# Optimization experiments

Measured on AMD Instinct MI355X. Metric: run time of the kernel, lower is better.

The kernel has to match this reference:

```python
import jax, jax.numpy as jnp
import numpy as np

N_NODES = 100000
N_EDGES = 1600000
D_FEAT = 128
N_CLASSES = 2
K_HOPS = 2


def setup_inputs() -> dict:
    key = jax.random.key(0)
    k1, k2, k3, k4 = jax.random.split(key, 4)
    x = jax.random.normal(k1, (N_NODES, D_FEAT), dtype=jnp.float32)
    edge_index = jax.random.randint(k2, (2, N_EDGES), 0, N_NODES, dtype=jnp.int64)
    weight = jax.random.normal(k3, (N_CLASSES, D_FEAT), dtype=jnp.float32) * (1.0 / np.sqrt(D_FEAT))
    bias = jnp.zeros((N_CLASSES,), dtype=jnp.float32)
    return {"x": x, "edge_index": edge_index, "weight": weight, "bias": bias}


def reference(x, edge_index, weight, bias):
    N = x.shape[0]
    # gcn_norm with self-loops (PyG SGConv default)
    loop = jnp.arange(N, dtype=edge_index.dtype)
    row = jnp.concatenate([edge_index[0], loop])  # source nodes
    col = jnp.concatenate([edge_index[1], loop])  # target nodes
    ones = jnp.ones(row.shape[0], dtype=x.dtype)
    deg = jax.ops.segment_sum(ones, col, num_segments=N)
    dinv = jnp.where(deg > 0, jax.lax.rsqrt(deg), 0.0)
    norm = dinv[row] * dinv[col]  # [E+N]

    # K hops of normalized sparse propagation: x <- A_norm @ x
    for _ in range(K_HOPS):
        x = jax.ops.segment_sum(x[row] * norm[:, None], col, num_segments=N)

    logits = x @ weight.T + bias  # [N, num_classes]
    return jax.nn.log_softmax(logits, axis=1)
```

## Files before the change

kernel.cpp:

```cpp
#include <hip/hip_runtime.h>

#define D_FEAT 128
#define BSH    8
#define BNODES 256
#define MAXNB  400
#define NSEG   512
#define SEGCAP 16
#define SENT   0xFFFFFFFFu
#define OVPB   16
#define MVB    2048
#define HTB    1024

typedef unsigned u32x4 __attribute__((ext_vector_type(4)));

__global__ __launch_bounds__(256) void k_fused(const float* __restrict__ x,
                                               const int* __restrict__ row,
                                               const int* __restrict__ col,
                                               const float* __restrict__ w,
                                               unsigned long long* __restrict__ ovbuf,
                                               unsigned* __restrict__ gbuf,
                                               float2* __restrict__ zvec,
                                               int E, int n, int NB) {
    __shared__ unsigned lcnt[MAXNB];
    __shared__ unsigned lbuf[MAXNB * SEGCAP];
    __shared__ unsigned lov;
    const int blk = blockIdx.x, tid = threadIdx.x;

    if (blk < NSEG) {
        for (int i = tid; i < NB; i += 256) lcnt[i] = 0;
        if (tid == 0) lov = 0;
        __syncthreads();

        const int chunk = (E + NSEG - 1) / NSEG;
        const int s = blk * chunk;
        const int e_end = min(s + chunk, E);
        for (int e = s + tid; e < e_end; e += 256) {
            int r = row[e], c = col[e];
            int b = c >> BSH;
            unsigned pos = atomicAdd(&lcnt[b], 1u);
            if (pos < SEGCAP) {
                lbuf[b * SEGCAP + pos] = ((unsigned)r << BSH) | (unsigned)(c & (BNODES - 1));
            } else {
                unsigned gi = atomicAdd(&lov, 1u);
                if (gi < OVPB)
                    ovbuf[(size_t)blk * OVPB + gi] =
                        ((unsigned long long)(unsigned)r << 32) | (unsigned)c;
            }
        }
        __syncthreads();

        if (tid < OVPB) {
            unsigned used = lov; if (used > OVPB) used = OVPB;
            if ((unsigned)tid >= used)
                ovbuf[(size_t)blk * OVPB + tid] = ~0ull;
        }

        const int total4 = NB * (SEGCAP / 4);
        uint4* g4 = (uint4*)gbuf;
        for (int idx = tid; idx < total4; idx += 256) {
            int b = idx >> 2, sg = (idx & 3) * 4;
            unsigned c2 = lcnt[b]; if (c2 > SEGCAP) c2 = SEGCAP;
            const unsigned* lb = &lbuf[b * SEGCAP + sg];
            uint4 v;
            v.x = ((unsigned)(sg + 0) < c2) ? lb[0] : SENT;
            v.y = ((unsigned)(sg + 1) < c2) ? lb[1] : SENT;
            v.z = ((unsigned)(sg + 2) < c2) ? lb[2] : SENT;
            v.w = ((unsigned)(sg + 3) < c2) ? lb[3] : SENT;
            g4[(((size_t)b * NSEG + blk) * SEGCAP + sg) >> 2] = v;
        }
    } else {
        const int lane = tid & 63;
        const float2 w0 = *(const float2*)(w + 2 * lane);
        const float2 w1 = *(const float2*)(w + D_FEAT + 2 * lane);
        const int wave0 = ((blk - NSEG) * 256 + tid) >> 6;
        const int nwaves = (MVB * 256) >> 6;
        for (int node = wave0; node < n; node += nwaves) {
            const float2 xv = *(const float2*)(x + (size_t)node * D_FEAT + 2 * lane);
            float p0 = xv.x * w0.x + xv.y * w0.y;
            float p1 = xv.x * w1.x + xv.y * w1.y;
            #pragma unroll
            for (int off = 32; off > 0; off >>= 1) {
                p0 += __shfl_down(p0, off, 64);
                p1 += __shfl_down(p1, off, 64);
            }
            if (lane == 0) zvec[node] = make_float2(p0, p1);
        }
    }
}

__global__ __launch_bounds__(HTB) void k_degnode(const unsigned* __restrict__ gbuf,
                                                 const unsigned long long* __restrict__ ovbuf,
                                                 const float2* __restrict__ z,
                                                 float* __restrict__ dinv,
                                                 float2* __restrict__ zd, int n) {
    __shared__ unsigned hist[BNODES];
    const int b = blockIdx.x, tid = threadIdx.x;
    if (tid < BNODES) hist[tid] = 0u;
    __syncthreads();

    const u32x4* p4 = (const u32x4*)(gbuf + (size_t)b * NSEG * SEGCAP);
    const int NIT = (NSEG * SEGCAP / 4) / HTB;
    #pragma unroll
    for (int k = 0; k < NIT; ++k) {
        u32x4 v = __builtin_nontemporal_load(p4 + tid + k * HTB);
        #pragma unroll
        for (int q = 0; q < 4; ++q)
            if (v[q] != SENT) atomicAdd(&hist[v[q] & (BNODES - 1)], 1u);
    }
    const int OVTOT = NSEG * OVPB;
    for (int i = tid; i < OVTOT; i += HTB) {
        unsigned long long e = ovbuf[i];
        unsigned c = (unsigned)e;
        if ((int)(c >> BSH) == b) atomicAdd(&hist[c & (BNODES - 1)], 1u);
    }
    __syncthreads();

    if (tid < BNODES) {
        int c = (b << BSH) + tid;
        if (c < n) {
            float d = rsqrtf((float)hist[tid] + 1.0f);
            dinv[c] = d;
            float2 zi = z[c];
            zd[c] = make_float2(zi.x * d, zi.y * d);
        }
    }
}

__global__ __launch_bounds__(HTB) void k_hop(const unsigned* __restrict__ gbuf,
                                             const unsigned long long* __restrict__ ovbuf,
                                             const float2* __restrict__ vin,
                                             const float* __restrict__ dinv,
                                             const float* __restrict__ bias,
                                             float2* __restrict__ outv,
                                             int n, int mode) {
    __shared__ float accx[BNODES];
    __shared__ float accy[BNODES];
    const int b = blockIdx.x, tid = threadIdx.x;
    if (tid < BNODES) { accx[tid] = 0.f; accy[tid] = 0.f; }
    __syncthreads();

    const u32x4* p4 = (const u32x4*)(gbuf + (size_t)b * NSEG * SEGCAP);
    const int NIT = (NSEG * SEGCAP / 4) / HTB;
    u32x4 vv[NIT];
    #pragma unroll
    for (int k = 0; k < NIT; ++k)
        vv[k] = __builtin_nontemporal_load(p4 + tid + k * HTB);

    #pragma unroll
    for (int k = 0; k < NIT; ++k) {
        u32x4 v = vv[k];
        #pragma unroll
        for (int q = 0; q < 4; ++q) {
            unsigned ent = v[q];
            if (ent != SENT) {
                float2 s = vin[ent >> BSH];
                atomicAdd(&accx[ent & (BNODES - 1)], s.x);
                atomicAdd(&accy[ent & (BNODES - 1)], s.y);
            }
        }
    }

    const int OVTOT = NSEG * OVPB;
    for (int i = tid; i < OVTOT; i += HTB) {
        unsigned long long e = ovbuf[i];
        unsigned c = (unsigned)e;
        if ((int)(c >> BSH) == b) {
            float2 s = vin[e >> 32];
            atomicAdd(&accx[c & (BNODES - 1)], s.x);
            atomicAdd(&accy[c & (BNODES - 1)], s.y);
        }
    }
    __syncthreads();

    if (tid < BNODES) {
        int c = (b << BSH) + tid;
        if (c < n) {
            float d = dinv[c];
            float2 s = vin[c];
            float ax = s.x + accx[tid];
            float ay = s.y + accy[tid];
            if (mode == 0) {
                float dd = d * d;
                outv[c] = make_float2(ax * dd, ay * dd);
            } else {
                float l0 = ax * d + bias[0];
                float l1 = ay * d + bias[1];
                float mx = fmaxf(l0, l1);
                float lse = mx + logf(expf(l0 - mx) + expf(l1 - mx));
                outv[c] = make_float2(l0 - lse, l1 - lse);
            }
        }
    }
}


__global__ __launch_bounds__(256) void k_matvec(const float* __restrict__ x,
                                                const float* __restrict__ w,
                                                float2* __restrict__ z, int n) {
    int wave = (int)((blockIdx.x * blockDim.x + threadIdx.x) >> 6);
    int lane = threadIdx.x & 63;
    if (wave >= n) return;
    const float2 xv = *(const float2*)(x + (size_t)wave * D_FEAT + 2 * lane);
    const float2 w0 = *(const float2*)(w + 2 * lane);
    const float2 w1 = *(const float2*)(w + D_FEAT + 2 * lane);
    float p0 = xv.x * w0.x + xv.y * w0.y;
    float p1 = xv.x * w1.x + xv.y * w1.y;
    #pragma unroll
    for (int off = 32; off > 0; off >>= 1) {
        p0 += __shfl_down(p0, off, 64);
        p1 += __shfl_down(p1, off, 64);
    }
    if (lane == 0) z[wave] = make_float2(p0, p1);
}

__global__ __launch_bounds__(256) void k_deg(const int* __restrict__ col,
                                             unsigned int* __restrict__ deg, int E) {
    int e = blockIdx.x * blockDim.x + threadIdx.x;
    if (e < E) atomicAdd(&deg[col[e]], 1u);
}

__global__ __launch_bounds__(256) void k_dinv_init(const unsigned int* __restrict__ deg,
                                                   float* __restrict__ dinv,
                                                   const float2* __restrict__ zin,
                                                   float2* __restrict__ yout, int n) {
    int i = blockIdx.x * blockDim.x + threadIdx.x;
    if (i < n) {
        float d = rsqrtf((float)deg[i] + 1.0f);
        dinv[i] = d;
        float2 zi = zin[i];
        float dd = d * d;
        yout[i] = make_float2(zi.x * dd, zi.y * dd);
    }
}

__global__ __launch_bounds__(256) void k_selfloop(const float* __restrict__ dinv,
                                                  const float2* __restrict__ zin,
                                                  float2* __restrict__ yout, int n) {
    int i = blockIdx.x * blockDim.x + threadIdx.x;
    if (i < n) {
        float d = dinv[i];
        float dd = d * d;
        float2 zi = zin[i];
        yout[i] = make_float2(zi.x * dd, zi.y * dd);
    }
}

__global__ __launch_bounds__(256) void k_edge(const int* __restrict__ row,
                                              const int* __restrict__ col,
                                              const float* __restrict__ dinv,
                                              const float2* __restrict__ zin,
                                              float* __restrict__ yout, int E) {
    int e = blockIdx.x * blockDim.x + threadIdx.x;
    if (e < E) {
        int r = row[e], c = col[e];
        float nr = dinv[r] * dinv[c];
        float2 zr = zin[r];
        atomicAdd(&yout[2 * c + 0], zr.x * nr);
        atomicAdd(&yout[2 * c + 1], zr.y * nr);
    }
}

__global__ __launch_bounds__(256) void k_final(const float2* __restrict__ y,
                                               const float* __restrict__ bias,
                                               float2* __restrict__ out, int n) {
    int i = blockIdx.x * blockDim.x + threadIdx.x;
    if (i < n) {
        float2 l = y[i];
        float l0 = l.x + bias[0];
        float l1 = l.y + bias[1];
        float m = fmaxf(l0, l1);
        float lse = m + logf(expf(l0 - m) + expf(l1 - m));
        out[i] = make_float2(l0 - lse, l1 - lse);
    }
}

extern "C" void kernel_launch(void* const* d_in, const int* in_sizes, int n_in,
                              void* d_out, int out_size, void* d_ws, size_t ws_size,
                              hipStream_t stream) {
    const float* x    = (const float*)d_in[0];
    const int*   ei   = (const int*)d_in[1];
    const float* w    = (const float*)d_in[2];
    const float* bias = (const float*)d_in[3];

    const int n = in_sizes[0] / D_FEAT;
    const int E = in_sizes[1] / 2;
    const int* row = ei;
    const int* col = ei + E;

    const int TB = 256;
    const int nodeBlocks = (n + TB - 1) / TB;
    const int edgeBlocks = (E + TB - 1) / TB;
    const int waveBlocks = (n + 3) / 4;

    const int NB = (n + BNODES - 1) >> BSH;

    size_t need = (size_t)NSEG * OVPB * 8
                + (size_t)NB * NSEG * SEGCAP * 4
                + (size_t)n * 8 * 3
                + (size_t)n * 4;

    if (NB <= MAXNB && n < (1 << 24) && ws_size >= need) {
        char* ws = (char*)d_ws;
        unsigned long long* ovbuf = (unsigned long long*)ws; ws += (size_t)NSEG * OVPB * 8;
        unsigned* gbuf = (unsigned*)ws;                      ws += (size_t)NB * NSEG * SEGCAP * 4;
        float2* zvec   = (float2*)ws;                        ws += (size_t)n * 8;
        float2* zd     = (float2*)ws;                        ws += (size_t)n * 8;
        float2* y1d    = (float2*)ws;                        ws += (size_t)n * 8;
        float*  dinv   = (float*)ws;

        k_fused  <<<NSEG + MVB, TB, 0, stream>>>(x, row, col, w, ovbuf, gbuf,
                                                 zvec, E, n, NB);
        k_degnode<<<NB, HTB, 0, stream>>>(gbuf, ovbuf, zvec, dinv, zd, n);
        k_hop    <<<NB, HTB, 0, stream>>>(gbuf, ovbuf, zd, dinv, bias, y1d, n, 0);
        k_hop    <<<NB, HTB, 0, stream>>>(gbuf, ovbuf, y1d, dinv, bias,
                                          (float2*)d_out, n, 1);
    } else {
        char* ws = (char*)d_ws;
        float2* z   = (float2*)ws; ws += (size_t)n * sizeof(float2);
        float2* y1  = (float2*)ws; ws += (size_t)n * sizeof(float2);
        float2* y2  = (float2*)ws; ws += (size_t)n * sizeof(float2);
        float*  dinv = (float*)ws; ws += (size_t)n * sizeof(float);
        unsigned int* deg = (unsigned int*)ws;

        (void)hipMemsetAsync(deg, 0, (size_t)n * sizeof(unsigned int), stream);
        k_deg<<<edgeBlocks, TB, 0, stream>>>(col, deg, E);
        k_matvec<<<waveBlocks, TB, 0, stream>>>(x, w, z, n);
        k_dinv_init<<<nodeBlocks, TB, 0, stream>>>(deg, dinv, z, y1, n);
        k_edge<<<edgeBlocks, TB, 0, stream>>>(row, col, dinv, z, (float*)y1, E);
        k_selfloop<<<nodeBlocks, TB, 0, stream>>>(dinv, y1, y2, n);
        k_edge<<<edgeBlocks, TB, 0, stream>>>(row, col, dinv, y1, (float*)y2, E);
        k_final<<<nodeBlocks, TB, 0, stream>>>(y2, bias, (float2*)d_out, n);
    }
}
```

Before: 165.6 us.

## Fuse bucketing, degree and both hops into one cooperative kernel

Replaces the four kernel launches with a single cooperative kernel of NB blocks that uses grid-wide syncs between the bucketing/matvec, degree, and two propagation phases. The edge partitioning now uses NB segments instead of a fixed 512, with segment capacity and overflow slots per segment enlarged to match. This removes the inter-kernel launch gaps and the tail effects of separate launches. In exchange it runs on only NB blocks of 512 threads (about 391), so parallelism in the bucketing and hop phases is lower, and it adds grid barrier costs. Overflow capacity is still bounded, so correctness depends on per-segment bucket counts staying within the new limits.

```diff
diff --git a/kernel.cpp b/kernel.cpp
--- a/kernel.cpp
+++ b/kernel.cpp
@@ -1,79 +1,92 @@
 #include <hip/hip_runtime.h>
+#include <hip/hip_cooperative_groups.h>
+
+namespace cg = cooperative_groups;
 
 #define D_FEAT 128
 #define BSH    8
 #define BNODES 256
 #define MAXNB  400
-#define NSEG   512
-#define SEGCAP 16
+#define SEGCAP 20
 #define SENT   0xFFFFFFFFu
-#define OVPB   16
-#define MVB    2048
-#define HTB    1024
+#define OVPB   32
+#define CTB    512
 
 typedef unsigned u32x4 __attribute__((ext_vector_type(4)));
 
-__global__ __launch_bounds__(256) void k_fused(const float* __restrict__ x,
-                                               const int* __restrict__ row,
-                                               const int* __restrict__ col,
-                                               const float* __restrict__ w,
-                                               unsigned long long* __restrict__ ovbuf,
-                                               unsigned* __restrict__ gbuf,
-                                               float2* __restrict__ zvec,
-                                               int E, int n, int NB) {
+__global__ __launch_bounds__(CTB, 4) void k_all(const float* __restrict__ x,
+                                                const int* __restrict__ row,
+                                                const int* __restrict__ col,
+                                                const float* __restrict__ w,
+                                                const float* __restrict__ bias,
+                                                unsigned long long* __restrict__ ovbuf,
+                                                unsigned* __restrict__ gbuf,
+                                                float2* __restrict__ zvec,
+                                                float2* __restrict__ zd,
+                                                float2* __restrict__ y1d,
+                                                float* __restrict__ dinv,
+                                                float2* __restrict__ out,
+                                                int E, int n, int NB) {
     __shared__ unsigned lcnt[MAXNB];
     __shared__ unsigned lbuf[MAXNB * SEGCAP];
     __shared__ unsigned lov;
+    __shared__ float accx[BNODES];
+    __shared__ float accy[BNODES];
+
+    cg::grid_group grid = cg::this_grid();
     const int blk = blockIdx.x, tid = threadIdx.x;
-
-    if (blk < NSEG) {
-        for (int i = tid; i < NB; i += 256) lcnt[i] = 0;
-        if (tid == 0) lov = 0;
-        __syncthreads();
-
-        const int chunk = (E + NSEG - 1) / NSEG;
-        const int s = blk * chunk;
-        const int e_end = min(s + chunk, E);
-        for (int e = s + tid; e < e_end; e += 256) {
-            int r = row[e], c = col[e];
-            int b = c >> BSH;
-            unsigned pos = atomicAdd(&lcnt[b], 1u);
-            if (pos < SEGCAP) {
-                lbuf[b * SEGCAP + pos] = ((unsigned)r << BSH) | (unsigned)(c & (BNODES - 1));
-            } else {
-                unsigned gi = atomicAdd(&lov, 1u);
-                if (gi < OVPB)
-                    ovbuf[(size_t)blk * OVPB + gi] =
-                        ((unsigned long long)(unsigned)r << 32) | (unsigned)c;
-            }
-        }
-        __syncthreads();
-
-        if (tid < OVPB) {
-            unsigned used = lov; if (used > OVPB) used = OVPB;
-            if ((unsigned)tid >= used)
-                ovbuf[(size_t)blk * OVPB + tid] = ~0ull;
-        }
-
+    const int b = blk;
+
+    for (int i = tid; i < NB; i += CTB) lcnt[i] = 0;
+    if (tid == 0) lov = 0;
+    __syncthreads();
+
+    const int chunk = (E + NB - 1) / NB;
+    const int s = blk * chunk;
+    const int e_end = min(s + chunk, E);
+    for (int e = s + tid; e < e_end; e += CTB) {
+        int r = row[e], c = col[e];
+        int bb = c >> BSH;
+        unsigned pos = atomicAdd(&lcnt[bb], 1u);
+        if (pos < SEGCAP) {
+            lbuf[bb * SEGCAP + pos] = ((unsigned)r << BSH) | (unsigned)(c & (BNODES - 1));
+        } else {
+            unsigned gi = atomicAdd(&lov, 1u);
+            if (gi < OVPB)
+                ovbuf[(size_t)blk * OVPB + gi] =
+                    ((unsigned long long)(unsigned)r << 32) | (unsigned)c;
+        }
+    }
+    __syncthreads();
+
+    if (tid < OVPB) {
+        unsigned used = lov; if (used > OVPB) used = OVPB;
+        if ((unsigned)tid >= used)
+            ovbuf[(size_t)blk * OVPB + tid] = ~0ull;
+    }
+
+    {
         const int total4 = NB * (SEGCAP / 4);
         uint4* g4 = (uint4*)gbuf;
-        for (int idx = tid; idx < total4; idx += 256) {
-            int b = idx >> 2, sg = (idx & 3) * 4;
-            unsigned c2 = lcnt[b]; if (c2 > SEGCAP) c2 = SEGCAP;
-            const unsigned* lb = &lbuf[b * SEGCAP + sg];
+        for (int idx = tid; idx < total4; idx += CTB) {
+            int bb = idx / 5, sg = (idx % 5) * 4;
+            unsigned c2 = lcnt[bb]; if (c2 > SEGCAP) c2 = SEGCAP;
+            const unsigned* lb = &lbuf[bb * SEGCAP + sg];
             uint4 v;
             v.x = ((unsigned)(sg + 0) < c2) ? lb[0] : SENT;
             v.y = ((unsigned)(sg + 1) < c2) ? lb[1] : SENT;
             v.z = ((unsigned)(sg + 2) < c2) ? lb[2] : SENT;
             v.w = ((unsigned)(sg + 3) < c2) ? lb[3] : SENT;
-            g4[(((size_t)b * NSEG + blk) * SEGCAP + sg) >> 2] = v;
-        }
-    } else {
+            g4[(((size_t)bb * NB + blk) * SEGCAP + sg) >> 2] = v;
+        }
+    }
+
+    {
         const int lane = tid & 63;
         const float2 w0 = *(const float2*)(w + 2 * lane);
         const float2 w1 = *(const float2*)(w + D_FEAT + 2 * lane);
-        const int wave0 = ((blk - NSEG) * 256 + tid) >> 6;
-        const int nwaves = (MVB * 256) >> 6;
+        const int wave0 = (blk * CTB + tid) >> 6;
+        const int nwaves = (NB * CTB) >> 6;
         for (int node = wave0; node < n; node += nwaves) {
             const float2 xv = *(const float2*)(x + (size_t)node * D_FEAT + 2 * lane);
             float p0 = xv.x * w0.x + xv.y * w0.y;
@@ -86,88 +99,97 @@
             if (lane == 0) zvec[node] = make_float2(p0, p1);
         }
     }
-}
-
-__global__ __launch_bounds__(HTB) void k_degnode(const unsigned* __restrict__ gbuf,
-                                                 const unsigned long long* __restrict__ ovbuf,
-                                                 const float2* __restrict__ z,
-                                                 float* __restrict__ dinv,
-                                                 float2* __restrict__ zd, int n) {
-    __shared__ unsigned hist[BNODES];
-    const int b = blockIdx.x, tid = threadIdx.x;
-    if (tid < BNODES) hist[tid] = 0u;
-    __syncthreads();
-
-    const u32x4* p4 = (const u32x4*)(gbuf + (size_t)b * NSEG * SEGCAP);
-    const int NIT = (NSEG * SEGCAP / 4) / HTB;
-    #pragma unroll
-    for (int k = 0; k < NIT; ++k) {
-        u32x4 v = __builtin_nontemporal_load(p4 + tid + k * HTB);
+    __threadfence();
+    grid.sync();
+
+    if (tid < BNODES) lcnt[tid] = 0u;
+    __syncthreads();
+
+    const u32x4* p4 = (const u32x4*)(gbuf + (size_t)b * NB * SEGCAP);
+    const int n4 = NB * (SEGCAP / 4);
+    for (int idx = tid; idx < n4; idx += CTB) {
+        u32x4 v = p4[idx];
         #pragma unroll
         for (int q = 0; q < 4; ++q)
-            if (v[q] != SENT) atomicAdd(&hist[v[q] & (BNODES - 1)], 1u);
-    }
-    const int OVTOT = NSEG * OVPB;
-    for (int i = tid; i < OVTOT; i += HTB) {
+            if (v[q] != SENT) atomicAdd(&lcnt[v[q] & (BNODES - 1)], 1u);
+    }
+    const int OVTOT = NB * OVPB;
+    for (int i = tid; i < OVTOT; i += CTB) {
         unsigned long long e = ovbuf[i];
         unsigned c = (unsigned)e;
-        if ((int)(c >> BSH) == b) atomicAdd(&hist[c & (BNODES - 1)], 1u);
+        if ((int)(c >> BSH) == b) atomicAdd(&lcnt[c & (BNODES - 1)], 1u);
     }
     __syncthreads();
 
     if (tid < BNODES) {
         int c = (b << BSH) + tid;
         if (c < n) {
-            float d = rsqrtf((float)hist[tid] + 1.0f);
+            float d = rsqrtf((float)lcnt[tid] + 1.0f);
             dinv[c] = d;
-            float2 zi = z[c];
+            float2 zi = zvec[c];
             zd[c] = make_float2(zi.x * d, zi.y * d);
         }
     }
-}
-
-__global__ __launch_bounds__(HTB) void k_hop(const unsigned* __restrict__ gbuf,
-                                             const unsigned long long* __restrict__ ovbuf,
-                                             const float2* __restrict__ vin,
-                                             const float* __restrict__ dinv,
-                                             const float* __restrict__ bias,
-                                             float2* __restrict__ outv,
-                                             int n, int mode) {
-    __shared__ float accx[BNODES];
-    __shared__ float accy[BNODES];
-    const int b = blockIdx.x, tid = threadIdx.x;
+    __threadfence();
+    grid.sync();
+
     if (tid < BNODES) { accx[tid] = 0.f; accy[tid] = 0.f; }
     __syncthreads();
-
-    const u32x4* p4 = (const u32x4*)(gbuf + (size_t)b * NSEG * SEGCAP);
-    const int NIT = (NSEG * SEGCAP / 4) / HTB;
-    u32x4 vv[NIT];
-    #pragma unroll
-    for (int k = 0; k < NIT; ++k)
-        vv[k] = __builtin_nontemporal_load(p4 + tid + k * HTB);
-
-    #pragma unroll
-    for (int k = 0; k < NIT; ++k) {
-        u32x4 v = vv[k];
+    for (int idx = tid; idx < n4; idx += CTB) {
+        u32x4 v = p4[idx];
         #pragma unroll
         for (int q = 0; q < 4; ++q) {
             unsigned ent = v[q];
             if (ent != SENT) {
-                float2 s = vin[ent >> BSH];
-                atomicAdd(&accx[ent & (BNODES - 1)], s.x);
-                atomicAdd(&accy[ent & (BNODES - 1)], s.y);
+                float2 sv = zd[ent >> BSH];
+                atomicAdd(&accx[ent & (BNODES - 1)], sv.x);
+                atomicAdd(&accy[ent & (BNODES - 1)], sv.y);
             }
         }
     }
-
-    const int OVTOT = NSEG * OVPB;
-    for (int i = tid; i < OVTOT; i += HTB) {
+    for (int i = tid; i < OVTOT; i += CTB) {
         unsigned long long e = ovbuf[i];
         unsigned c = (unsigned)e;
         if ((int)(c >> BSH) == b) {
-            float2 s = vin[e >> 32];
-            atomicAdd(&accx[c & (BNODES - 1)], s.x);
-            atomicAdd(&accy[c & (BNODES - 1)], s.y);
+            float2 sv = zd[e >> 32];
+            atomicAdd(&accx[c & (BNODES - 1)], sv.x);
+            atomicAdd(&accy[c & (BNODES - 1)], sv.y);
+        }
+    }
+    __syncthreads();
+
+    if (tid < BNODES) {
+        int c = (b << BSH) + tid;
+        if (c < n) {
+            float d = dinv[c], dd = d * d;
+            float2 sv = zd[c];
+            y1d[c] = make_float2((sv.x + accx[tid]) * dd, (sv.y + accy[tid]) * dd);
+        }
+    }
+    __threadfence();
+    grid.sync();
+
+    if (tid < BNODES) { accx[tid] = 0.f; accy[tid] = 0.f; }
+    __syncthreads();
+    for (int idx = tid; idx < n4; idx += CTB) {
+        u32x4 v = p4[idx];
+        #pragma unroll
+        for (int q = 0; q < 4; ++q) {
+            unsigned ent = v[q];
+            if (ent != SENT) {
+                float2 sv = y1d[ent >> BSH];
+                atomicAdd(&accx[ent & (BNODES - 1)], sv.x);
+                atomicAdd(&accy[ent & (BNODES - 1)], sv.y);
+            }
+        }
+    }
+    for (int i = tid; i < OVTOT; i += CTB) {
+        unsigned long long e = ovbuf[i];
+        unsigned c = (unsigned)e;
+        if ((int)(c >> BSH) == b) {
+            float2 sv = y1d[e >> 32];
+            atomicAdd(&accx[c & (BNODES - 1)], sv.x);
+            atomicAdd(&accy[c & (BNODES - 1)], sv.y);
         }
     }
     __syncthreads();
@@ -176,19 +198,12 @@
         int c = (b << BSH) + tid;
         if (c < n) {
             float d = dinv[c];
-            float2 s = vin[c];
-            float ax = s.x + accx[tid];
-            float ay = s.y + accy[tid];
-            if (mode == 0) {
-                float dd = d * d;
-                outv[c] = make_float2(ax * dd, ay * dd);
-            } else {
-                float l0 = ax * d + bias[0];
-                float l1 = ay * d + bias[1];
-                float mx = fmaxf(l0, l1);
-                float lse = mx + logf(expf(l0 - mx) + expf(l1 - mx));
-                outv[c] = make_float2(l0 - lse, l1 - lse);
-            }
+            float2 sv = y1d[c];
+            float l0 = (sv.x + accx[tid]) * d + bias[0];
+            float l1 = (sv.y + accy[tid]) * d + bias[1];
+            float mx = fmaxf(l0, l1);
+            float lse = mx + logf(expf(l0 - mx) + expf(l1 - mx));
+            out[c] = make_float2(l0 - lse, l1 - lse);
         }
     }
 }
@@ -294,26 +309,29 @@
 
     const int NB = (n + BNODES - 1) >> BSH;
 
-    size_t need = (size_t)NSEG * OVPB * 8
-                + (size_t)NB * NSEG * SEGCAP * 4
+    size_t need = (size_t)NB * OVPB * 8
+                + (size_t)NB * NB * SEGCAP * 4
                 + (size_t)n * 8 * 3
                 + (size_t)n * 4;
 
     if (NB <= MAXNB && n < (1 << 24) && ws_size >= need) {
         char* ws = (char*)d_ws;
-        unsigned long long* ovbuf = (unsigned long long*)ws; ws += (size_t)NSEG * OVPB * 8;
-        unsigned* gbuf = (unsigned*)ws;                      ws += (size_t)NB * NSEG * SEGCAP * 4;
+        unsigned long long* ovbuf = (unsigned long long*)ws; ws += (size_t)NB * OVPB * 8;
+        unsigned* gbuf = (unsigned*)ws;                      ws += (size_t)NB * NB * SEGCAP * 4;
         float2* zvec   = (float2*)ws;                        ws += (size_t)n * 8;
         float2* zd     = (float2*)ws;                        ws += (size_t)n * 8;
         float2* y1d    = (float2*)ws;                        ws += (size_t)n * 8;
         float*  dinv   = (float*)ws;
 
-        k_fused  <<<NSEG + MVB, TB, 0, stream>>>(x, row, col, w, ovbuf, gbuf,
-                                                 zvec, E, n, NB);
-        k_degnode<<<NB, HTB, 0, stream>>>(gbuf, ovbuf, zvec, dinv, zd, n);
-        k_hop    <<<NB, HTB, 0, stream>>>(gbuf, ovbuf, zd, dinv, bias, y1d, n, 0);
-        k_hop    <<<NB, HTB, 0, stream>>>(gbuf, ovbuf, y1d, dinv, bias,
-                                          (float2*)d_out, n, 1);
+        float2* outp = (float2*)d_out;
+        int En = E, nn = n, nb = NB;
+        void* args[] = {
+            (void*)&x, (void*)&row, (void*)&col, (void*)&w, (void*)&bias,
+            (void*)&ovbuf, (void*)&gbuf, (void*)&zvec, (void*)&zd, (void*)&y1d,
+            (void*)&dinv, (void*)&outp, (void*)&En, (void*)&nn, (void*)&nb
+        };
+        (void)hipLaunchCooperativeKernel((void*)k_all, dim3(NB), dim3(CTB),
+                                         args, 0, stream);
     } else {
         char* ws = (char*)d_ws;
         float2* z   = (float2*)ws; ws += (size_t)n * sizeof(float2);
```

New measurement: 501.5 us. +202.7%, slower.
